# Optimization experiments

Measured on AMD Instinct MI355X. Metric: run time of the kernel, lower is better.

Reference implementation:

```python
import jax, jax.numpy as jnp
import numpy as np

H = 8  # head_count


def setup_inputs() -> dict:
    key = jax.random.key(0)
    ks = jax.random.split(key, 9)
    n, C, w = 8, 512, 8192
    Kc, Vc = 512, 512
    s = 0.02
    return {
        "x": jax.random.normal(ks[0], (n, C, w), dtype=jnp.float32),
        "Wk": jax.random.normal(ks[1], (Kc, C), dtype=jnp.float32) * s,
        "bk": jax.random.normal(ks[2], (Kc,), dtype=jnp.float32) * s,
        "Wq": jax.random.normal(ks[3], (Kc, C), dtype=jnp.float32) * s,
        "bq": jax.random.normal(ks[4], (Kc,), dtype=jnp.float32) * s,
        "Wv": jax.random.normal(ks[5], (Vc, C), dtype=jnp.float32) * s,
        "bv": jax.random.normal(ks[6], (Vc,), dtype=jnp.float32) * s,
        "Wr": jax.random.normal(ks[7], (C, Vc), dtype=jnp.float32) * s,
        "br": jax.random.normal(ks[8], (C,), dtype=jnp.float32) * s,
    }


def reference(x, Wk, bk, Wq, bq, Wv, bv, Wr, br):
    n, C, w = x.shape
    Kc, Vc = Wk.shape[0], Wv.shape[0]
    hk, hv = Kc // H, Vc // H
    # 1x1 Conv1d == channel-mixing GEMM
    keys = jnp.einsum('kc,ncw->nkw', Wk, x) + bk[None, :, None]
    queries = jnp.einsum('kc,ncw->nkw', Wq, x) + bq[None, :, None]
    values = jnp.einsum('vc,ncw->nvw', Wv, x) + bv[None, :, None]
    # split heads: [n, H, hd, w]
    K = jax.nn.softmax(keys.reshape(n, H, hk, w), axis=-1)   # softmax over positions
    Q = jax.nn.softmax(queries.reshape(n, H, hk, w), axis=2)  # softmax over channels
    V = values.reshape(n, H, hv, w)
    # context = K @ V^T : [n, H, hk, hv]
    ctx = jnp.einsum('nhkw,nhvw->nhkv', K, V)
    # attended = ctx^T @ Q : [n, H, hv, w]
    att = jnp.einsum('nhkv,nhkw->nhvw', ctx, Q).reshape(n, Vc, w)
    out = jnp.einsum('cv,nvw->ncw', Wr, att) + br[None, :, None] + x
    return out
```

## Files before the change

### kernel.cpp

```cpp
#include <hip/hip_runtime.h>
#include <hip/hip_bf16.h>
#include <cstdint>

#define NB 8
#define CD 512
#define WD 8192
#define NH 8

typedef __bf16 bf16x8 __attribute__((ext_vector_type(8)));
typedef float  f32x4  __attribute__((ext_vector_type(4)));

__device__ __forceinline__ void gload_lds16(const __bf16* g, __bf16* l) {
  __builtin_amdgcn_global_load_lds((const __attribute__((address_space(1))) void*)g,
                                   (__attribute__((address_space(3))) void*)l,
                                   16, 0, 0);
}

__global__ void __launch_bounds__(256) prep_x_kernel(const float* __restrict__ x,
                                                     __bf16* __restrict__ xT) {
  __shared__ float tile[64][65];
  const int n = blockIdx.z, cb = blockIdx.y * 64, wb = blockIdx.x * 64;
  const int t = threadIdx.x;
  const int t63 = t & 63, tg = t >> 6;
  const float* xp = x + ((size_t)n * CD + cb) * WD + wb;
#pragma unroll
  for (int i = 0; i < 16; i++) {
    const int cc = tg * 16 + i;
    tile[cc][t63] = xp[(size_t)cc * WD + t63];
  }
  __syncthreads();
  __bf16* op = xT + ((size_t)n * WD + wb) * CD + cb;
#pragma unroll
  for (int i = 0; i < 16; i++) {
    const int ww = tg * 16 + i;
    op[(size_t)ww * CD + t63] = (__bf16)tile[t63][ww];
  }
}

__global__ void __launch_bounds__(256) prep_w_kernel(const float* __restrict__ Wk,
                                                     const float* __restrict__ Wq,
                                                     const float* __restrict__ Wv,
                                                     const float* __restrict__ Wr,
                                                     const float* __restrict__ bk,
                                                     const float* __restrict__ bv,
                                                     __bf16* __restrict__ WkvB,
                                                     __bf16* __restrict__ WqB,
                                                     __bf16* __restrict__ WrB,
                                                     float* __restrict__ bkv) {
  const int gid = blockIdx.x * 256 + threadIdx.x;
  WkvB[gid]          = (__bf16)Wk[gid];
  WkvB[262144 + gid] = (__bf16)Wv[gid];
  WqB[gid]           = (__bf16)Wq[gid];
  WrB[gid]           = (__bf16)Wr[gid];
  if (gid < 512)       bkv[gid] = bk[gid];
  else if (gid < 1024) bkv[gid] = bv[gid - 512];
}

__device__ __forceinline__ void gemm_lds_core(const __bf16* __restrict__ A,
                                              const __bf16* __restrict__ B,
                                              f32x4 (&acc)[4][4], __bf16* lds) {
  const int t = threadIdx.x;
  const int lane = t & 63, wave = t >> 6;
  const int l15 = lane & 15, quad = lane >> 4;
  const int wm = (wave >> 1) << 6, wn = (wave & 1) << 6;
#pragma unroll 1
  for (int kc = 0; kc < 8; kc++) {
    const __bf16* Ak = A + kc * 64;
    const __bf16* Bk = B + kc * 64;
#pragma unroll
    for (int rnd = 0; rnd < 8; rnd++) {
      const int c = rnd * 256 + t;
      const int cc = c & 1023;
      const int r = cc >> 3;
      const int g = (cc & 7) ^ (r & 7);
      const __bf16* src = ((c >> 10) ? Bk : Ak) + (size_t)r * 512 + g * 8;
      gload_lds16(src, lds + (size_t)c * 8);
    }
    __syncthreads();
#pragma unroll
    for (int k0 = 0; k0 < 2; k0++) {
      const int gk = k0 * 4 + quad;
      bf16x8 av[4], bv[4];
#pragma unroll
      for (int i = 0; i < 4; i++) {
        const int r = wm + i * 16 + l15;
        av[i] = *(const bf16x8*)(lds + (size_t)((r << 3) + (gk ^ (r & 7))) * 8);
      }
#pragma unroll
      for (int j = 0; j < 4; j++) {
        const int r = wn + j * 16 + l15;
        bv[j] = *(const bf16x8*)(lds + (size_t)(8192 + (r << 3) + (gk ^ (r & 7))) * 8);
      }
#pragma unroll
      for (int i = 0; i < 4; i++)
#pragma unroll
        for (int j = 0; j < 4; j++)
          acc[i][j] = __builtin_amdgcn_mfma_f32_16x16x32_bf16(av[i], bv[j], acc[i][j], 0, 0, 0);
    }
    __syncthreads();
  }
}

__global__ void __launch_bounds__(256) gemm_kv_kernel(const __bf16* __restrict__ WkvB,
                                                      const __bf16* __restrict__ xT,
                                                      const float* __restrict__ bkv,
                                                      __bf16* __restrict__ kv) {
  __shared__ __bf16 lds[16384];
  const int n = blockIdx.z, m0 = blockIdx.y * 128, w0 = blockIdx.x * 128;
  f32x4 acc[4][4];
#pragma unroll
  for (int i = 0; i < 4; i++)
#pragma unroll
    for (int j = 0; j < 4; j++) acc[i][j] = (f32x4){0.f, 0.f, 0.f, 0.f};
  gemm_lds_core(WkvB + (size_t)m0 * 512, xT + ((size_t)n * WD + w0) * 512, acc, lds);
  const int t = threadIdx.x, lane = t & 63, wave = t >> 6;
  const int l15 = lane & 15, quad = lane >> 4;
  const int wm = (wave >> 1) << 6, wn = (wave & 1) << 6;
  __bf16* outp = kv + (size_t)n * 1024 * WD;
#pragma unroll
  for (int i = 0; i < 4; i++)
#pragma unroll
    for (int j = 0; j < 4; j++)
#pragma unroll
      for (int r = 0; r < 4; r++) {
        const int m = m0 + wm + i * 16 + quad * 4 + r;
        const int w = w0 + wn + j * 16 + l15;
        outp[(size_t)m * WD + w] = (__bf16)(acc[i][j][r] + bkv[m]);
      }
}

__global__ void __launch_bounds__(256) gemm_qT_kernel(const __bf16* __restrict__ xT,
                                                      const __bf16* __restrict__ WqB,
                                                      const float* __restrict__ bq,
                                                      __bf16* __restrict__ qT) {
  __shared__ __bf16 lds[16384];
  const int n = blockIdx.z, w0 = blockIdx.x * 128, q0 = blockIdx.y * 128;
  f32x4 acc[4][4];
#pragma unroll
  for (int i = 0; i < 4; i++)
#pragma unroll
    for (int j = 0; j < 4; j++) acc[i][j] = (f32x4){0.f, 0.f, 0.f, 0.f};
  gemm_lds_core(xT + ((size_t)n * WD + w0) * 512, WqB + (size_t)q0 * 512, acc, lds);
  const int t = threadIdx.x, lane = t & 63, wave = t >> 6;
  const int l15 = lane & 15, quad = lane >> 4;
  const int wm = (wave >> 1) << 6, wn = (wave & 1) << 6;
#pragma unroll
  for (int i = 0; i < 4; i++)
#pragma unroll
    for (int j = 0; j < 4; j++)
#pragma unroll
      for (int r = 0; r < 4; r++) {
        const int w = w0 + wm + i * 16 + quad * 4 + r;
        const int kq = q0 + wn + j * 16 + l15;
        qT[((size_t)n * WD + w) * 512 + kq] = (__bf16)(acc[i][j][r] + bq[kq]);
      }
}

__global__ void __launch_bounds__(256) gemm_out_kernel(const __bf16* __restrict__ Mf,
                                                       const __bf16* __restrict__ qT,
                                                       const float* __restrict__ br,
                                                       const float* __restrict__ x,
                                                       float* __restrict__ out) {
  __shared__ __bf16 lds[16384];
  const int n = blockIdx.z, c0 = blockIdx.y * 128, w0 = blockIdx.x * 128;
  f32x4 acc[4][4];
#pragma unroll
  for (int i = 0; i < 4; i++)
#pragma unroll
    for (int j = 0; j < 4; j++) acc[i][j] = (f32x4){0.f, 0.f, 0.f, 0.f};
  gemm_lds_core(Mf + ((size_t)n * 512 + c0) * 512, qT + ((size_t)n * WD + w0) * 512, acc, lds);
  const int t = threadIdx.x, lane = t & 63, wave = t >> 6;
  const int l15 = lane & 15, quad = lane >> 4;
  const int wm = (wave >> 1) << 6, wn = (wave & 1) << 6;
#pragma unroll
  for (int i = 0; i < 4; i++)
#pragma unroll
    for (int j = 0; j < 4; j++)
#pragma unroll
      for (int r = 0; r < 4; r++) {
        const int c = c0 + wm + i * 16 + quad * 4 + r;
        const int w = w0 + wn + j * 16 + l15;
        const size_t idx = ((size_t)n * CD + c) * WD + w;
        out[idx] = acc[i][j][r] + br[c] + x[idx];
      }
}

__global__ void __launch_bounds__(256) kstats_kernel(const __bf16* __restrict__ kv,
                                                     float* __restrict__ kmax,
                                                     float* __restrict__ kinv) {
  const int row = blockIdx.x;
  const int n = row >> 9, k = row & 511;
  const __bf16* p = kv + ((size_t)n * 1024 + k) * WD;
  const int t = threadIdx.x, lane = t & 63, wave = t >> 6;
  float v[32];
#pragma unroll
  for (int i = 0; i < 4; i++) {
    bf16x8 d = *(const bf16x8*)(p + (size_t)(t + i * 256) * 8);
#pragma unroll
    for (int e = 0; e < 8; e++) v[i * 8 + e] = (float)d[e];
  }
  float mx = v[0];
#pragma unroll
  for (int i = 1; i < 32; i++) mx = fmaxf(mx, v[i]);
#pragma unroll
  for (int off = 32; off > 0; off >>= 1) mx = fmaxf(mx, __shfl_down(mx, off));
  __shared__ float red[8];
  if (lane == 0) red[wave] = mx;
  __syncthreads();
  mx = fmaxf(fmaxf(red[0], red[1]), fmaxf(red[2], red[3]));
  float s = 0.f;
#pragma unroll
  for (int i = 0; i < 32; i++) s += __expf(v[i] - mx);
#pragma unroll
  for (int off = 32; off > 0; off >>= 1) s += __shfl_down(s, off);
  if (lane == 0) red[4 + wave] = s;
  __syncthreads();
  if (t == 0) {
    kmax[row] = mx;
    kinv[row] = 1.0f / (red[4] + red[5] + red[6] + red[7]);
  }
}

__global__ void __launch_bounds__(256) qsm_kernel(__bf16* __restrict__ qT) {
  const int gid = blockIdx.x * 256 + threadIdx.x;
  const int h = gid & 7;
  const int w = (gid >> 3) & 8191;
  const int n = gid >> 16;
  __bf16* p = qT + ((size_t)n * WD + w) * 512 + h * 64;
  float v[64];
#pragma unroll
  for (int c = 0; c < 8; c++) {
    bf16x8 d = *(const bf16x8*)(p + c * 8);
#pragma unroll
    for (int e = 0; e < 8; e++) v[c * 8 + e] = (float)d[e];
  }
  float mx = v[0];
#pragma unroll
  for (int i = 1; i < 64; i++) mx = fmaxf(mx, v[i]);
  float s = 0.f;
#pragma unroll
  for (int i = 0; i < 64; i++) { v[i] = __expf(v[i] - mx); s += v[i]; }
  const float inv = 1.0f / s;
#pragma unroll
  for (int c = 0; c < 8; c++) {
    bf16x8 o;
#pragma unroll
    for (int e = 0; e < 8; e++) o[e] = (__bf16)(v[c * 8 + e] * inv);
    *(bf16x8*)(p + c * 8) = o;
  }
}

__global__ void __launch_bounds__(256) ctx_kernel(const __bf16* __restrict__ kv,
                                                  const float* __restrict__ kmax,
                                                  const float* __restrict__ kinv,
                                                  float* __restrict__ partial) {
  const int chunk = blockIdx.x, h = blockIdx.y, n = blockIdx.z;
  const int t = threadIdx.x, lane = t & 63, wave = t >> 6;
  const int l15 = lane & 15, quad = lane >> 4;
  const int krow = h * 64 + wave * 16 + l15;
  const float sm = kmax[n * 512 + krow];
  const float si = kinv[n * 512 + krow];
  const __bf16* Kp = kv + ((size_t)n * 1024 + krow) * WD + chunk * 1024 + quad * 8;
  const __bf16* Vp = kv + ((size_t)n * 1024 + 512 + h * 64 + l15) * WD + chunk * 1024 + quad * 8;
  f32x4 acc[4];
#pragma unroll
  for (int j = 0; j < 4; j++) acc[j] = (f32x4){0.f, 0.f, 0.f, 0.f};
  for (int s = 0; s < 32; s++) {
    bf16x8 kraw = *(const bf16x8*)(Kp + s * 32);
    bf16x8 af;
#pragma unroll
    for (int e = 0; e < 8; e++) af[e] = (__bf16)(__expf((float)kraw[e] - sm) * si);
#pragma unroll
    for (int j = 0; j < 4; j++) {
      bf16x8 bv = *(const bf16x8*)(Vp + (size_t)(j * 16) * WD + s * 32);
      acc[j] = __builtin_amdgcn_mfma_f32_16x16x32_bf16(af, bv, acc[j], 0, 0, 0);
    }
  }
  float* pp = partial + (((size_t)(n * 8 + h) * 8 + chunk) << 12);
#pragma unroll
  for (int j = 0; j < 4; j++)
#pragma unroll
    for (int r = 0; r < 4; r++) {
      const int kr = wave * 16 + quad * 4 + r;
      const int vc = j * 16 + l15;
      pp[kr * 64 + vc] = acc[j][r];
    }
}

__global__ void __launch_bounds__(256) ctx_reduce_kernel(const float* __restrict__ partial,
                                                         __bf16* __restrict__ ctxB) {
  const int gid = blockIdx.x * 256 + threadIdx.x;
  const int nh = gid >> 12;
  const int kvi = gid & 4095;
  const float* pp = partial + ((size_t)nh << 15) + kvi;
  float s = 0.f;
#pragma unroll
  for (int c = 0; c < 8; c++) s += pp[(size_t)c << 12];
  ctxB[gid] = (__bf16)s;
}

__global__ void __launch_bounds__(256) mfuse_kernel(const __bf16* __restrict__ WrB,
                                                    const __bf16* __restrict__ ctxB,
                                                    __bf16* __restrict__ Mf) {
  const int ms = blockIdx.x, h = blockIdx.y, n = blockIdx.z;
  const int t = threadIdx.x, lane = t & 63, wave = t >> 6;
  const int l15 = lane & 15, quad = lane >> 4;
  f32x4 acc[2][4];
#pragma unroll
  for (int i = 0; i < 2; i++)
#pragma unroll
    for (int j = 0; j < 4; j++) acc[i][j] = (f32x4){0.f, 0.f, 0.f, 0.f};
  const __bf16* Ap = WrB + (size_t)(ms * 128 + wave * 32 + l15) * 512 + h * 64 + quad * 8;
  const __bf16* Bp = ctxB + ((size_t)(n * 8 + h) << 12) + (size_t)l15 * 64 + quad * 8;
#pragma unroll
  for (int k0 = 0; k0 < 64; k0 += 32) {
    bf16x8 av[2];
#pragma unroll
    for (int i = 0; i < 2; i++) av[i] = *(const bf16x8*)(Ap + i * 16 * 512 + k0);
#pragma unroll
    for (int j = 0; j < 4; j++) {
      bf16x8 bv = *(const bf16x8*)(Bp + j * 16 * 64 + k0);
#pragma unroll
      for (int i = 0; i < 2; i++)
        acc[i][j] = __builtin_amdgcn_mfma_f32_16x16x32_bf16(av[i], bv, acc[i][j], 0, 0, 0);
    }
  }
#pragma unroll
  for (int i = 0; i < 2; i++)
#pragma unroll
    for (int j = 0; j < 4; j++)
#pragma unroll
      for (int r = 0; r < 4; r++) {
        const int c = ms * 128 + wave * 32 + i * 16 + quad * 4 + r;
        const int col = h * 64 + j * 16 + l15;
        Mf[((size_t)n * 512 + c) * 512 + col] = (__bf16)acc[i][j][r];
      }
}

extern "C" void kernel_launch(void* const* d_in, const int* in_sizes, int n_in,
                              void* d_out, int out_size, void* d_ws, size_t ws_size,
                              hipStream_t stream) {
  (void)in_sizes; (void)n_in; (void)out_size; (void)ws_size;
  const float* x  = (const float*)d_in[0];
  const float* Wk = (const float*)d_in[1];
  const float* bk = (const float*)d_in[2];
  const float* Wq = (const float*)d_in[3];
  const float* bq = (const float*)d_in[4];
  const float* Wv = (const float*)d_in[5];
  const float* bv = (const float*)d_in[6];
  const float* Wr = (const float*)d_in[7];
  const float* br = (const float*)d_in[8];
  float* out = (float*)d_out;

  char* ws = (char*)d_ws;
  __bf16* xT      = (__bf16*)ws;
  float*  partial = (float*)ws;
  __bf16* ctxB    = (__bf16*)(ws + (16ull << 20));
  __bf16* Mf      = (__bf16*)(ws + (20ull << 20));
  __bf16* kv      = (__bf16*)(ws + (64ull << 20));
  __bf16* qT      = (__bf16*)(ws + (192ull << 20));

  char* scr = (char*)d_out + (124ull << 20);
  __bf16* WkvB = (__bf16*)scr;
  __bf16* WqB  = (__bf16*)(scr + (1ull << 20));
  __bf16* WrB  = (__bf16*)(scr + (1536ull << 10));
  float*  bkv  = (float*)(scr + (2ull << 20));
  float*  kmaxp = (float*)(scr + (2ull << 20) + 16384);
  float*  kinvp = (float*)(scr + (2ull << 20) + 32768);

  prep_x_kernel<<<dim3(128, 8, 8), 256, 0, stream>>>(x, xT);
  prep_w_kernel<<<dim3(1024), 256, 0, stream>>>(Wk, Wq, Wv, Wr, bk, bv, WkvB, WqB, WrB, bkv);
  gemm_kv_kernel<<<dim3(64, 8, 8), 256, 0, stream>>>(WkvB, xT, bkv, kv);
  gemm_qT_kernel<<<dim3(64, 4, 8), 256, 0, stream>>>(xT, WqB, bq, qT);
  kstats_kernel<<<dim3(4096), 256, 0, stream>>>(kv, kmaxp, kinvp);
  qsm_kernel<<<dim3(2048), 256, 0, stream>>>(qT);
  ctx_kernel<<<dim3(8, 8, 8), 256, 0, stream>>>(kv, kmaxp, kinvp, partial);
  ctx_reduce_kernel<<<dim3(1024), 256, 0, stream>>>(partial, ctxB);
  mfuse_kernel<<<dim3(4, 8, 8), 256, 0, stream>>>(WrB, ctxB, Mf);
  gemm_out_kernel<<<dim3(64, 4, 8), 256, 0, stream>>>(Mf, qT, br, x, out);
}
```

Measured before the change: 550.5 us.

## Fuse softmaxes into GEMM/ctx kernels and switch GEMMs to 32x32 MFMA

The query softmax moves into the gemm_qT epilogue, reduced across the 64-channel head with lane shuffles, so the separate qsm pass over qT is gone. The key softmax drops the max-subtraction. ctx_kernel now accumulates exp sums and ctx_reduce divides by them, which removes the kstats pass over K. The kv and out GEMMs switch to 32x32x16 MFMA with a reworked epilogue. Skipping the max-subtraction risks overflow for large logits, and accuracy now relies on the small input scale.

After: 501.8 us. -8.8%, faster.

```diff
diff --git a/kernel.cpp b/kernel.cpp
--- a/kernel.cpp
+++ b/kernel.cpp
@@ -9,6 +9,7 @@
 
 typedef __bf16 bf16x8 __attribute__((ext_vector_type(8)));
 typedef float  f32x4  __attribute__((ext_vector_type(4)));
+typedef float  f32x16 __attribute__((ext_vector_type(16)));
 
 __device__ __forceinline__ void gload_lds16(const __bf16* g, __bf16* l) {
   __builtin_amdgcn_global_load_lds((const __attribute__((address_space(1))) void*)g,
@@ -56,6 +57,16 @@
   else if (gid < 1024) bkv[gid] = bv[gid - 512];
 }
 
+#define STAGE_SLAB(Ak, Bk, lds, t)                                          \
+  _Pragma("unroll") for (int rnd = 0; rnd < 8; rnd++) {                     \
+    const int c = rnd * 256 + (t);                                          \
+    const int cc = c & 1023;                                                \
+    const int r = cc >> 3;                                                  \
+    const int g = (cc & 7) ^ (r & 7);                                       \
+    const __bf16* src = ((c >> 10) ? (Bk) : (Ak)) + (size_t)r * 512 + g * 8;\
+    gload_lds16(src, (lds) + (size_t)c * 8);                                \
+  }
+
 __device__ __forceinline__ void gemm_lds_core(const __bf16* __restrict__ A,
                                               const __bf16* __restrict__ B,
                                               f32x4 (&acc)[4][4], __bf16* lds) {
@@ -67,15 +78,7 @@
   for (int kc = 0; kc < 8; kc++) {
     const __bf16* Ak = A + kc * 64;
     const __bf16* Bk = B + kc * 64;
-#pragma unroll
-    for (int rnd = 0; rnd < 8; rnd++) {
-      const int c = rnd * 256 + t;
-      const int cc = c & 1023;
-      const int r = cc >> 3;
-      const int g = (cc & 7) ^ (r & 7);
-      const __bf16* src = ((c >> 10) ? Bk : Ak) + (size_t)r * 512 + g * 8;
-      gload_lds16(src, lds + (size_t)c * 8);
-    }
+    STAGE_SLAB(Ak, Bk, lds, t)
     __syncthreads();
 #pragma unroll
     for (int k0 = 0; k0 < 2; k0++) {
@@ -96,6 +99,43 @@
 #pragma unroll
         for (int j = 0; j < 4; j++)
           acc[i][j] = __builtin_amdgcn_mfma_f32_16x16x32_bf16(av[i], bv[j], acc[i][j], 0, 0, 0);
+    }
+    __syncthreads();
+  }
+}
+
+__device__ __forceinline__ void gemm_lds_core32(const __bf16* __restrict__ A,
+                                                const __bf16* __restrict__ B,
+                                                f32x16 (&acc)[2][2], __bf16* lds) {
+  const int t = threadIdx.x;
+  const int lane = t & 63, wave = t >> 6;
+  const int l31 = lane & 31, khalf = lane >> 5;
+  const int wm = (wave >> 1) << 6, wn = (wave & 1) << 6;
+#pragma unroll 1
+  for (int kc = 0; kc < 8; kc++) {
+    const __bf16* Ak = A + kc * 64;
+    const __bf16* Bk = B + kc * 64;
+    STAGE_SLAB(Ak, Bk, lds, t)
+    __syncthreads();
+#pragma unroll
+    for (int kk = 0; kk < 4; kk++) {
+      const int g = kk * 2 + khalf;
+      bf16x8 av[2], bv[2];
+#pragma unroll
+      for (int i = 0; i < 2; i++) {
+        const int r = wm + i * 32 + l31;
+        av[i] = *(const bf16x8*)(lds + (size_t)((r << 3) + (g ^ (r & 7))) * 8);
+      }
+#pragma unroll
+      for (int j = 0; j < 2; j++) {
+        const int r = wn + j * 32 + l31;
+        bv[j] = *(const bf16x8*)(lds + (size_t)(8192 + (r << 3) + (g ^ (r & 7))) * 8);
+      }
+#pragma unroll
+      for (int i = 0; i < 2; i++)
+#pragma unroll
+        for (int j = 0; j < 2; j++)
+          acc[i][j] = __builtin_amdgcn_mfma_f32_32x32x16_bf16(av[i], bv[j], acc[i][j], 0, 0, 0);
     }
     __syncthreads();
   }
@@ -107,26 +147,29 @@
                                                       __bf16* __restrict__ kv) {
   __shared__ __bf16 lds[16384];
   const int n = blockIdx.z, m0 = blockIdx.y * 128, w0 = blockIdx.x * 128;
-  f32x4 acc[4][4];
-#pragma unroll
-  for (int i = 0; i < 4; i++)
-#pragma unroll
-    for (int j = 0; j < 4; j++) acc[i][j] = (f32x4){0.f, 0.f, 0.f, 0.f};
-  gemm_lds_core(WkvB + (size_t)m0 * 512, xT + ((size_t)n * WD + w0) * 512, acc, lds);
-  const int t = threadIdx.x, lane = t & 63, wave = t >> 6;
-  const int l15 = lane & 15, quad = lane >> 4;
-  const int wm = (wave >> 1) << 6, wn = (wave & 1) << 6;
-  __bf16* outp = kv + (size_t)n * 1024 * WD;
-#pragma unroll
-  for (int i = 0; i < 4; i++)
-#pragma unroll
-    for (int j = 0; j < 4; j++)
-#pragma unroll
-      for (int r = 0; r < 4; r++) {
-        const int m = m0 + wm + i * 16 + quad * 4 + r;
-        const int w = w0 + wn + j * 16 + l15;
-        outp[(size_t)m * WD + w] = (__bf16)(acc[i][j][r] + bkv[m]);
-      }
+  f32x16 acc[2][2];
+#pragma unroll
+  for (int i = 0; i < 2; i++)
+#pragma unroll
+    for (int j = 0; j < 2; j++)
+#pragma unroll
+      for (int r = 0; r < 16; r++) acc[i][j][r] = 0.f;
+  gemm_lds_core32(WkvB + (size_t)m0 * 512, xT + ((size_t)n * WD + w0) * 512, acc, lds);
+  const int t = threadIdx.x, lane = t & 63, wave = t >> 6;
+  const int l31 = lane & 31, khalf = lane >> 5;
+  const int wm = (wave >> 1) << 6, wn = (wave & 1) << 6;
+  __bf16* outp = kv + (size_t)n * 1024 * WD + w0 + wn + l31;
+#pragma unroll
+  for (int i = 0; i < 2; i++)
+#pragma unroll
+    for (int reg = 0; reg < 16; reg++) {
+      const int row = (reg & 3) + 8 * (reg >> 2) + 4 * khalf;
+      const int m = m0 + wm + i * 32 + row;
+      const float bias = bkv[m];
+      __bf16* rp = outp + (size_t)m * WD;
+#pragma unroll
+      for (int j = 0; j < 2; j++) rp[j * 32] = (__bf16)(acc[i][j][reg] + bias);
+    }
 }
 
 __global__ void __launch_bounds__(256) gemm_qT_kernel(const __bf16* __restrict__ xT,
@@ -144,16 +187,30 @@
   const int t = threadIdx.x, lane = t & 63, wave = t >> 6;
   const int l15 = lane & 15, quad = lane >> 4;
   const int wm = (wave >> 1) << 6, wn = (wave & 1) << 6;
+  float bqv[4];
+#pragma unroll
+  for (int j = 0; j < 4; j++) bqv[j] = bq[q0 + wn + j * 16 + l15];
 #pragma unroll
   for (int i = 0; i < 4; i++)
 #pragma unroll
-    for (int j = 0; j < 4; j++)
-#pragma unroll
-      for (int r = 0; r < 4; r++) {
-        const int w = w0 + wm + i * 16 + quad * 4 + r;
-        const int kq = q0 + wn + j * 16 + l15;
-        qT[((size_t)n * WD + w) * 512 + kq] = (__bf16)(acc[i][j][r] + bq[kq]);
-      }
+    for (int r = 0; r < 4; r++) {
+      float e[4];
+      float s = 0.f;
+#pragma unroll
+      for (int j = 0; j < 4; j++) {
+        e[j] = __expf(acc[i][j][r] + bqv[j]);
+        s += e[j];
+      }
+      s += __shfl_xor(s, 1);
+      s += __shfl_xor(s, 2);
+      s += __shfl_xor(s, 4);
+      s += __shfl_xor(s, 8);
+      const float inv = 1.0f / s;
+      const int w = w0 + wm + i * 16 + quad * 4 + r;
+      __bf16* rp = qT + ((size_t)n * WD + w) * 512 + q0 + wn + l15;
+#pragma unroll
+      for (int j = 0; j < 4; j++) rp[j * 16] = (__bf16)(e[j] * inv);
+    }
 }
 
 __global__ void __launch_bounds__(256) gemm_out_kernel(const __bf16* __restrict__ Mf,
@@ -163,119 +220,61 @@
                                                        float* __restrict__ out) {
   __shared__ __bf16 lds[16384];
   const int n = blockIdx.z, c0 = blockIdx.y * 128, w0 = blockIdx.x * 128;
-  f32x4 acc[4][4];
-#pragma unroll
-  for (int i = 0; i < 4; i++)
-#pragma unroll
-    for (int j = 0; j < 4; j++) acc[i][j] = (f32x4){0.f, 0.f, 0.f, 0.f};
-  gemm_lds_core(Mf + ((size_t)n * 512 + c0) * 512, qT + ((size_t)n * WD + w0) * 512, acc, lds);
-  const int t = threadIdx.x, lane = t & 63, wave = t >> 6;
-  const int l15 = lane & 15, quad = lane >> 4;
-  const int wm = (wave >> 1) << 6, wn = (wave & 1) << 6;
-#pragma unroll
-  for (int i = 0; i < 4; i++)
-#pragma unroll
-    for (int j = 0; j < 4; j++)
-#pragma unroll
-      for (int r = 0; r < 4; r++) {
-        const int c = c0 + wm + i * 16 + quad * 4 + r;
-        const int w = w0 + wn + j * 16 + l15;
-        const size_t idx = ((size_t)n * CD + c) * WD + w;
-        out[idx] = acc[i][j][r] + br[c] + x[idx];
-      }
-}
-
-__global__ void __launch_bounds__(256) kstats_kernel(const __bf16* __restrict__ kv,
-                                                     float* __restrict__ kmax,
-                                                     float* __restrict__ kinv) {
-  const int row = blockIdx.x;
-  const int n = row >> 9, k = row & 511;
-  const __bf16* p = kv + ((size_t)n * 1024 + k) * WD;
-  const int t = threadIdx.x, lane = t & 63, wave = t >> 6;
-  float v[32];
-#pragma unroll
-  for (int i = 0; i < 4; i++) {
-    bf16x8 d = *(const bf16x8*)(p + (size_t)(t + i * 256) * 8);
-#pragma unroll
-    for (int e = 0; e < 8; e++) v[i * 8 + e] = (float)d[e];
-  }
-  float mx = v[0];
-#pragma unroll
-  for (int i = 1; i < 32; i++) mx = fmaxf(mx, v[i]);
-#pragma unroll
-  for (int off = 32; off > 0; off >>= 1) mx = fmaxf(mx, __shfl_down(mx, off));
-  __shared__ float red[8];
-  if (lane == 0) red[wave] = mx;
-  __syncthreads();
-  mx = fmaxf(fmaxf(red[0], red[1]), fmaxf(red[2], red[3]));
-  float s = 0.f;
-#pragma unroll
-  for (int i = 0; i < 32; i++) s += __expf(v[i] - mx);
-#pragma unroll
-  for (int off = 32; off > 0; off >>= 1) s += __shfl_down(s, off);
-  if (lane == 0) red[4 + wave] = s;
-  __syncthreads();
-  if (t == 0) {
-    kmax[row] = mx;
-    kinv[row] = 1.0f / (red[4] + red[5] + red[6] + red[7]);
-  }
-}
-
-__global__ void __launch_bounds__(256) qsm_kernel(__bf16* __restrict__ qT) {
-  const int gid = blockIdx.x * 256 + threadIdx.x;
-  const int h = gid & 7;
-  const int w = (gid >> 3) & 8191;
-  const int n = gid >> 16;
-  __bf16* p = qT + ((size_t)n * WD + w) * 512 + h * 64;
-  float v[64];
-#pragma unroll
-  for (int c = 0; c < 8; c++) {
-    bf16x8 d = *(const bf16x8*)(p + c * 8);
-#pragma unroll
-    for (int e = 0; e < 8; e++) v[c * 8 + e] = (float)d[e];
-  }
-  float mx = v[0];
-#pragma unroll
-  for (int i = 1; i < 64; i++) mx = fmaxf(mx, v[i]);
-  float s = 0.f;
-#pragma unroll
-  for (int i = 0; i < 64; i++) { v[i] = __expf(v[i] - mx); s += v[i]; }
-  const float inv = 1.0f / s;
-#pragma unroll
-  for (int c = 0; c < 8; c++) {
-    bf16x8 o;
-#pragma unroll
-    for (int e = 0; e < 8; e++) o[e] = (__bf16)(v[c * 8 + e] * inv);
-    *(bf16x8*)(p + c * 8) = o;
-  }
+  f32x16 acc[2][2];
+#pragma unroll
+  for (int i = 0; i < 2; i++)
+#pragma unroll
+    for (int j = 0; j < 2; j++)
+#pragma unroll
+      for (int r = 0; r < 16; r++) acc[i][j][r] = 0.f;
+  gemm_lds_core32(Mf + ((size_t)n * 512 + c0) * 512, qT + ((size_t)n * WD + w0) * 512, acc, lds);
+  const int t = threadIdx.x, lane = t & 63, wave = t >> 6;
+  const int l31 = lane & 31, khalf = lane >> 5;
+  const int wm = (wave >> 1) << 6, wn = (wave & 1) << 6;
+#pragma unroll
+  for (int i = 0; i < 2; i++)
+#pragma unroll
+    for (int reg = 0; reg < 16; reg++) {
+      const int row = (reg & 3) + 8 * (reg >> 2) + 4 * khalf;
+      const int c = c0 + wm + i * 32 + row;
+      const float bias = br[c];
+      const size_t base = ((size_t)n * CD + c) * WD + w0 + wn + l31;
+#pragma unroll
+      for (int j = 0; j < 2; j++)
+        out[base + j * 32] = acc[i][j][reg] + bias + x[base + j * 32];
+    }
 }
 
 __global__ void __launch_bounds__(256) ctx_kernel(const __bf16* __restrict__ kv,
-                                                  const float* __restrict__ kmax,
-                                                  const float* __restrict__ kinv,
-                                                  float* __restrict__ partial) {
+                                                  float* __restrict__ partial,
+                                                  float* __restrict__ ssum) {
   const int chunk = blockIdx.x, h = blockIdx.y, n = blockIdx.z;
   const int t = threadIdx.x, lane = t & 63, wave = t >> 6;
   const int l15 = lane & 15, quad = lane >> 4;
   const int krow = h * 64 + wave * 16 + l15;
-  const float sm = kmax[n * 512 + krow];
-  const float si = kinv[n * 512 + krow];
   const __bf16* Kp = kv + ((size_t)n * 1024 + krow) * WD + chunk * 1024 + quad * 8;
   const __bf16* Vp = kv + ((size_t)n * 1024 + 512 + h * 64 + l15) * WD + chunk * 1024 + quad * 8;
   f32x4 acc[4];
 #pragma unroll
   for (int j = 0; j < 4; j++) acc[j] = (f32x4){0.f, 0.f, 0.f, 0.f};
+  float esum = 0.f;
   for (int s = 0; s < 32; s++) {
     bf16x8 kraw = *(const bf16x8*)(Kp + s * 32);
     bf16x8 af;
 #pragma unroll
-    for (int e = 0; e < 8; e++) af[e] = (__bf16)(__expf((float)kraw[e] - sm) * si);
+    for (int e = 0; e < 8; e++) {
+      const float ev = __expf((float)kraw[e]);
+      esum += ev;
+      af[e] = (__bf16)ev;
+    }
 #pragma unroll
     for (int j = 0; j < 4; j++) {
       bf16x8 bv = *(const bf16x8*)(Vp + (size_t)(j * 16) * WD + s * 32);
       acc[j] = __builtin_amdgcn_mfma_f32_16x16x32_bf16(af, bv, acc[j], 0, 0, 0);
     }
   }
+  esum += __shfl_xor(esum, 16);
+  esum += __shfl_xor(esum, 32);
   float* pp = partial + (((size_t)(n * 8 + h) * 8 + chunk) << 12);
 #pragma unroll
   for (int j = 0; j < 4; j++)
@@ -285,18 +284,25 @@
       const int vc = j * 16 + l15;
       pp[kr * 64 + vc] = acc[j][r];
     }
+  if (lane < 16)
+    ssum[(((size_t)(n * 8 + h) * 8 + chunk) << 6) + wave * 16 + l15] = esum;
 }
 
 __global__ void __launch_bounds__(256) ctx_reduce_kernel(const float* __restrict__ partial,
+                                                         const float* __restrict__ ssum,
                                                          __bf16* __restrict__ ctxB) {
   const int gid = blockIdx.x * 256 + threadIdx.x;
   const int nh = gid >> 12;
   const int kvi = gid & 4095;
+  const int k = kvi >> 6;
+  float s = 0.f;
+#pragma unroll
+  for (int c = 0; c < 8; c++) s += ssum[(((size_t)nh * 8 + c) << 6) + k];
   const float* pp = partial + ((size_t)nh << 15) + kvi;
-  float s = 0.f;
-#pragma unroll
-  for (int c = 0; c < 8; c++) s += pp[(size_t)c << 12];
-  ctxB[gid] = (__bf16)s;
+  float v = 0.f;
+#pragma unroll
+  for (int c = 0; c < 8; c++) v += pp[(size_t)c << 12];
+  ctxB[gid] = (__bf16)(v / s);
 }
 
 __global__ void __launch_bounds__(256) mfuse_kernel(const __bf16* __restrict__ WrB,
@@ -365,17 +371,14 @@
   __bf16* WqB  = (__bf16*)(scr + (1ull << 20));
   __bf16* WrB  = (__bf16*)(scr + (1536ull << 10));
   float*  bkv  = (float*)(scr + (2ull << 20));
-  float*  kmaxp = (float*)(scr + (2ull << 20) + 16384);
-  float*  kinvp = (float*)(scr + (2ull << 20) + 32768);
+  float*  ssum = (float*)(scr + (2ull << 20) + 65536);
 
   prep_x_kernel<<<dim3(128, 8, 8), 256, 0, stream>>>(x, xT);
   prep_w_kernel<<<dim3(1024), 256, 0, stream>>>(Wk, Wq, Wv, Wr, bk, bv, WkvB, WqB, WrB, bkv);
   gemm_kv_kernel<<<dim3(64, 8, 8), 256, 0, stream>>>(WkvB, xT, bkv, kv);
   gemm_qT_kernel<<<dim3(64, 4, 8), 256, 0, stream>>>(xT, WqB, bq, qT);
-  kstats_kernel<<<dim3(4096), 256, 0, stream>>>(kv, kmaxp, kinvp);
-  qsm_kernel<<<dim3(2048), 256, 0, stream>>>(qT);
-  ctx_kernel<<<dim3(8, 8, 8), 256, 0, stream>>>(kv, kmaxp, kinvp, partial);
-  ctx_reduce_kernel<<<dim3(1024), 256, 0, stream>>>(partial, ctxB);
+  ctx_kernel<<<dim3(8, 8, 8), 256, 0, stream>>>(kv, partial, ssum);
+  ctx_reduce_kernel<<<dim3(1024), 256, 0, stream>>>(partial, ssum, ctxB);
   mfuse_kernel<<<dim3(4, 8, 8), 256, 0, stream>>>(WrB, ctxB, Mf);
   gemm_out_kernel<<<dim3(64, 4, 8), 256, 0, stream>>>(Mf, qT, br, x, out);
 }
```
